# Kernel optimization log

Hardware: AMD Instinct MI355X
Metric: run time of the kernel (lower is better)

Reference implementation:

```python
import jax, jax.numpy as jnp
import numpy as np

B, S, H = 2, 2048, 1024
NH, NKV, HD = 16, 4, 64
Q_SIZE = NH * HD          # 1024
KV_SIZE = NKV * HD        # 256
R_SOFTPLUS_0 = 1.442695041
NEG = -2.3819763e38  # large negative for masking (matches float32 -inf-ish additive mask)


def setup_inputs() -> dict:
    key = jax.random.key(0)
    k1, k2, k3, k4, k5, k6 = jax.random.split(key, 6)
    hidden_states = jax.random.normal(k1, (B, S, H), dtype=jnp.float32)
    # causal additive mask [B, 1, S, S]
    causal = jnp.tril(jnp.ones((S, S), dtype=bool))
    mask = jnp.where(causal, 0.0, NEG).astype(jnp.float32)
    mask = jnp.broadcast_to(mask[None, None], (B, 1, S, S))
    fan = 1.0 / np.sqrt(H)
    qkv_w = jax.random.uniform(k2, ((NH + 2 * NKV) * HD, H), jnp.float32, -fan, fan)
    qkv_b = jax.random.uniform(k3, ((NH + 2 * NKV) * HD,), jnp.float32, -fan, fan)
    fo = 1.0 / np.sqrt(Q_SIZE)
    o_w = jax.random.uniform(k4, (H, Q_SIZE), jnp.float32, -fo, fo)
    o_b = jax.random.uniform(k5, (H,), jnp.float32, -fo, fo)
    scaling = jax.random.normal(k6, (HD,), dtype=jnp.float32)
    return {"hidden_states": hidden_states, "mask": mask, "scaling": scaling,
            "qkv_w": qkv_w, "qkv_b": qkv_b, "o_w": o_w, "o_b": o_b}


def reference(hidden_states, mask, scaling, qkv_w, qkv_b, o_w, o_b):
    b, s, _ = hidden_states.shape
    q_w, k_w, v_w = qkv_w[:Q_SIZE], qkv_w[Q_SIZE:Q_SIZE + KV_SIZE], qkv_w[-KV_SIZE:]
    q_b, k_b, v_b = qkv_b[:Q_SIZE], qkv_b[Q_SIZE:Q_SIZE + KV_SIZE], qkv_b[-KV_SIZE:]
    xq = (hidden_states @ q_w.T + q_b).reshape(b, s, NH, HD)
    # per-dim softplus scaling fused into q
    scale = (R_SOFTPLUS_0 / np.sqrt(HD)) * jax.nn.softplus(scaling)
    xq = xq * scale[None, None, None, :]
    xk = (hidden_states @ k_w.T + k_b).reshape(b, s, NKV, HD)
    xv = (hidden_states @ v_w.T + v_b).reshape(b, s, NKV, HD)
    # GQA: repeat kv heads (repeat_interleave along head dim)
    key = jnp.repeat(xk, NH // NKV, axis=2)   # [b, s, NH, HD]
    value = jnp.repeat(xv, NH // NKV, axis=2)
    scores = jnp.einsum('bqhd,bkhd->bhqk', xq, key) + mask
    scores = jax.nn.softmax(scores.astype(jnp.float32), axis=-1).astype(xq.dtype)
    out = jnp.einsum('bhqk,bkhd->bqhd', scores, value).reshape(b, s, NH * HD)
    out = out @ o_w.T + o_b
    return scores, out
```

## Files before the change

### kernel.cpp

```cpp
#include <hip/hip_runtime.h>
#include <hip/hip_bf16.h>
#include <cstdint>
#include <cstddef>

typedef __attribute__((ext_vector_type(4))) float f32x4;
typedef __attribute__((ext_vector_type(8))) short bf16x8;

#define DEVI static __device__ __forceinline__

DEVI unsigned short f2bf(float f) {
  union { float f; unsigned int u; } v; v.f = f;
  unsigned int u = v.u;
  unsigned int r = (u + 0x7fffu + ((u >> 16) & 1u)) >> 16;
  return (unsigned short)r;
}

DEVI unsigned int cvt_pk(float lo, float hi) {
  unsigned int r;
  asm("v_cvt_pk_bf16_f32 %0, %1, %2" : "=v"(r) : "v"(lo), "v"(hi));
  return r;
}

DEVI f32x4 mfma16(bf16x8 a, bf16x8 b, f32x4 c) {
  return __builtin_amdgcn_mfma_f32_16x16x32_bf16(a, b, c, 0, 0, 0);
}

#define GLDS(gp, lp) __builtin_amdgcn_global_load_lds(                         \
    (const __attribute__((address_space(1))) void*)(const void*)(gp),          \
    (__attribute__((address_space(3))) void*)(void*)(lp), 16, 0, 0)

#define SBAR() asm volatile("s_barrier" ::: "memory")
#define WV(n) asm volatile("s_waitcnt vmcnt(" #n ")" ::: "memory")
#define FORCE4(x) asm volatile("" : "+v"(x))

__global__ void convert_kernel(const float* __restrict__ hidden,
                               const float* __restrict__ qkv_w,
                               const float* __restrict__ o_w,
                               const float* __restrict__ scaling,
                               unsigned short* __restrict__ hbf,
                               unsigned short* __restrict__ wbf,
                               unsigned short* __restrict__ obf,
                               float* __restrict__ qscale) {
  int tid = blockIdx.x * blockDim.x + threadIdx.x;
  int nt = gridDim.x * blockDim.x;
  if (tid < 64) {
    float x = scaling[tid];
    float sp = (x > 20.f) ? x : log1pf(__expf(x));
    qscale[tid] = 0.1803368801243369f * 1.4426950408889634f * sp;
  }
  for (int i = tid; i < 1048576; i += nt) {
    float4 v = ((const float4*)hidden)[i];
    ushort4 o = { f2bf(v.x), f2bf(v.y), f2bf(v.z), f2bf(v.w) };
    ((ushort4*)hbf)[i] = o;
  }
  for (int i = tid; i < 393216; i += nt) {
    float4 v = ((const float4*)qkv_w)[i];
    ushort4 o = { f2bf(v.x), f2bf(v.y), f2bf(v.z), f2bf(v.w) };
    ((ushort4*)wbf)[i] = o;
  }
  for (int i = tid; i < 262144; i += nt) {
    float4 v = ((const float4*)o_w)[i];
    ushort4 o = { f2bf(v.x), f2bf(v.y), f2bf(v.z), f2bf(v.w) };
    ((ushort4*)obf)[i] = o;
  }
}

__global__ __launch_bounds__(256, 2) void gemm_kernel(
    const unsigned short* __restrict__ A,
    const unsigned short* __restrict__ Bw,
    const float* __restrict__ bias,
    const float* __restrict__ qscale,
    unsigned short* __restrict__ oq,
    unsigned short* __restrict__ okv,
    unsigned short* __restrict__ ovt) {
  __shared__ __align__(16) unsigned short sA[128 * 64];
  __shared__ __align__(16) unsigned short sB[128 * 64];
  const int t = threadIdx.x, lane = t & 63, w = t >> 6;
  const int l15 = lane & 15, lg = lane >> 4;
  const int m0 = blockIdx.y * 128, n0 = blockIdx.x * 128;
  const int wr = w >> 1, wc = w & 1;

  f32x4 acc[4][4] = {};

  for (int kb = 0; kb < 1024; kb += 64) {
    __syncthreads();
#pragma unroll
    for (int i = 0; i < 4; i++) {
      int idx = i * 256 + w * 64 + lane;
      int row = idx >> 3;
      int cg = (idx & 7) ^ (row & 7);
      GLDS(A + (size_t)(m0 + row) * 1024 + kb + cg * 8, sA + (i * 256 + w * 64) * 8);
      GLDS(Bw + (size_t)(n0 + row) * 1024 + kb + cg * 8, sB + (i * 256 + w * 64) * 8);
    }
    __syncthreads();
    bf16x8 af[4][2], bfr[4][2];
#pragma unroll
    for (int rt = 0; rt < 4; rt++) {
      int row = wr * 64 + rt * 16 + l15;
#pragma unroll
      for (int kk = 0; kk < 2; kk++) {
        int c = (kk * 4 + lg) ^ (row & 7);
        af[rt][kk] = *(const bf16x8*)((const char*)sA + row * 128 + c * 16);
      }
      int rowb = wc * 64 + rt * 16 + l15;
#pragma unroll
      for (int kk = 0; kk < 2; kk++) {
        int c = (kk * 4 + lg) ^ (rowb & 7);
        bfr[rt][kk] = *(const bf16x8*)((const char*)sB + rowb * 128 + c * 16);
      }
    }
#pragma unroll
    for (int kk = 0; kk < 2; kk++)
#pragma unroll
      for (int rt = 0; rt < 4; rt++)
#pragma unroll
        for (int ct = 0; ct < 4; ct++)
          acc[rt][ct] = mfma16(af[rt][kk], bfr[ct][kk], acc[rt][ct]);
  }

#pragma unroll
  for (int rt = 0; rt < 4; rt++) {
#pragma unroll
    for (int ct = 0; ct < 4; ct++) {
      int n = n0 + wc * 64 + ct * 16 + l15;
      float bv = bias[n];
#pragma unroll
      for (int jj = 0; jj < 4; jj++) {
        int m = m0 + wr * 64 + rt * 16 + lg * 4 + jj;
        float v = acc[rt][ct][jj] + bv;
        int b = m >> 11, s = m & 2047;
        if (n < 1024) {
          int h = n >> 6, d = n & 63;
          v *= qscale[d];
          oq[(((size_t)(b * 16 + h) * 2048 + s) << 6) + d] = f2bf(v);
        } else if (n < 1280) {
          int kv = (n - 1024) >> 6, d = n & 63;
          okv[(((size_t)(b * 4 + kv) * 2048 + s) << 6) + d] = f2bf(v);
        } else {
          int kv = (n - 1280) >> 6, d = n & 63;
          ovt[(((size_t)((b * 4 + kv) * 64 + d)) << 11) + s] = f2bf(v);
        }
      }
    }
  }
}

__global__ __launch_bounds__(256, 2) void gemm2_kernel(
    const unsigned short* __restrict__ A,
    const unsigned short* __restrict__ Bw,
    const float* __restrict__ bias,
    float* __restrict__ of) {
  __shared__ __align__(16) unsigned short sA[64 * 64];
  __shared__ __align__(16) unsigned short sB[128 * 64];
  __shared__ __align__(16) float sT[4][32 * 68];
  const int t = threadIdx.x, lane = t & 63, w = t >> 6;
  const int l15 = lane & 15, lg = lane >> 4;
  const int m0 = blockIdx.y * 64, n0 = blockIdx.x * 128;
  const int wr = w >> 1, wc = w & 1;

  f32x4 acc[2][4] = {};

  for (int kb = 0; kb < 1024; kb += 64) {
    __syncthreads();
#pragma unroll
    for (int i = 0; i < 2; i++) {
      int idx = i * 256 + w * 64 + lane;
      int row = idx >> 3;
      int cg = (idx & 7) ^ (row & 7);
      GLDS(A + (size_t)(m0 + row) * 1024 + kb + cg * 8, sA + (i * 256 + w * 64) * 8);
    }
#pragma unroll
    for (int i = 0; i < 4; i++) {
      int idx = i * 256 + w * 64 + lane;
      int row = idx >> 3;
      int cg = (idx & 7) ^ (row & 7);
      GLDS(Bw + (size_t)(n0 + row) * 1024 + kb + cg * 8, sB + (i * 256 + w * 64) * 8);
    }
    __syncthreads();
    bf16x8 af[2][2], bfr[4][2];
#pragma unroll
    for (int rt = 0; rt < 2; rt++) {
      int row = wr * 32 + rt * 16 + l15;
#pragma unroll
      for (int kk = 0; kk < 2; kk++) {
        int c = (kk * 4 + lg) ^ (row & 7);
        af[rt][kk] = *(const bf16x8*)((const char*)sA + row * 128 + c * 16);
      }
    }
#pragma unroll
    for (int ct = 0; ct < 4; ct++) {
      int rowb = wc * 64 + ct * 16 + l15;
#pragma unroll
      for (int kk = 0; kk < 2; kk++) {
        int c = (kk * 4 + lg) ^ (rowb & 7);
        bfr[ct][kk] = *(const bf16x8*)((const char*)sB + rowb * 128 + c * 16);
      }
    }
#pragma unroll
    for (int kk = 0; kk < 2; kk++)
#pragma unroll
      for (int rt = 0; rt < 2; rt++)
#pragma unroll
        for (int ct = 0; ct < 4; ct++)
          acc[rt][ct] = mfma16(af[rt][kk], bfr[ct][kk], acc[rt][ct]);
  }

#pragma unroll
  for (int rt = 0; rt < 2; rt++)
#pragma unroll
    for (int ct = 0; ct < 4; ct++)
#pragma unroll
      for (int jj = 0; jj < 4; jj++) {
        int r = rt * 16 + lg * 4 + jj;
        int cc = ct * 16 + l15;
        sT[w][r * 68 + cc] = acc[rt][ct][jj];
      }
#pragma unroll
  for (int i = 0; i < 8; i++) {
    int r = i * 4 + lg;
    int cc = l15 * 4;
    f32x4 v = *(const f32x4*)&sT[w][r * 68 + cc];
    int n = n0 + wc * 64 + cc;
    float4 bv = *(const float4*)(bias + n);
    v[0] += bv.x; v[1] += bv.y; v[2] += bv.z; v[3] += bv.w;
    int m = m0 + wr * 32 + r;
    *(f32x4*)(of + (size_t)m * 1024 + n) = v;
  }
}

__global__ __launch_bounds__(256, 2) void attn_kernel(
    const unsigned short* __restrict__ q_ws,
    const unsigned short* __restrict__ k_ws,
    const unsigned short* __restrict__ v_ws,
    float* __restrict__ scores,
    unsigned short* __restrict__ attn_bf) {
  __shared__ __align__(16) unsigned char smem[57344];

  const int t = threadIdx.x, lane = t & 63, w = t >> 6;
  const int l15 = lane & 15, lg = lane >> 4;
  int bid = blockIdx.x;
  int bh = bid & 31;
  int pr = bid >> 5;
  int p = (bid < 256) ? pr : (23 - pr);
  int b = bh >> 4, h = bh & 15, kv = h >> 2;
  const int qtA = p, qtB = 31 - p;
  const int NB = qtB + 1;
  const int start = bid & 15;

  const unsigned short* Kp = k_ws + ((size_t)(b * 4 + kv) * 2048) * 64;
  const unsigned short* Vp = v_ws + ((size_t)(b * 4 + kv) * 64) * 2048;
  const int qrA = qtA * 64 + w * 16 + l15;
  const int qrB = qtB * 64 + w * 16 + l15;

  auto rot = [&](int j) { int n = j + start; return (n >= NB) ? n - NB : n; };
  auto kbuf = [&](int i) { return (unsigned short*)(smem + i * 8192); };
  auto vbuf = [&](int i) { return (unsigned short*)(smem + 32768 + i * 8192); };
  float* Sw = (float*)(smem + 16384 + w * 4096);
  unsigned char* myP = smem + 49152 + w * 2048;

  bf16x8 aqA[2], aqB[2];
  {
    const unsigned short* qa = q_ws + ((size_t)bh * 2048 + qrA) * 64;
    const unsigned short* qb = q_ws + ((size_t)bh * 2048 + qrB) * 64;
    aqA[0] = *(const bf16x8*)(qa + lg * 8);
    aqA[1] = *(const bf16x8*)(qa + 32 + lg * 8);
    aqB[0] = *(const bf16x8*)(qb + lg * 8);
    aqB[1] = *(const bf16x8*)(qb + 32 + lg * 8);
    FORCE4(*(f32x4*)&aqA[0]); FORCE4(*(f32x4*)&aqA[1]);
    FORCE4(*(f32x4*)&aqB[0]); FORCE4(*(f32x4*)&aqB[1]);
  }

  auto stageK = [&](int kt, int bufi) {
#pragma unroll
    for (int i = 0; i < 2; i++) {
      int idx = i * 256 + w * 64 + lane;
      int row = idx >> 3;
      int cg = (idx & 7) ^ (row & 7);
      GLDS(Kp + (size_t)(kt * 64 + row) * 64 + cg * 8, kbuf(bufi) + (i * 256 + w * 64) * 8);
    }
  };
  auto stageVT = [&](int kt, int bufi) {
#pragma unroll
    for (int i = 0; i < 2; i++) {
      int idx = i * 256 + w * 64 + lane;
      int row = idx >> 3;
      int cg = (idx & 7) ^ (row & 7);
      GLDS(Vp + (size_t)row * 2048 + kt * 64 + cg * 8, vbuf(bufi) + (i * 256 + w * 64) * 8);
    }
  };
  auto qk_tile = [&](const unsigned short* kb, const bf16x8(&aq)[2], f32x4(&acc)[4]) {
#pragma unroll
    for (int ct = 0; ct < 4; ct++) {
      int row = ct * 16 + l15;
#pragma unroll
      for (int kk = 0; kk < 2; kk++) {
        int c = (kk * 4 + lg) ^ (row & 7);
        bf16x8 ak = *(const bf16x8*)((const char*)kb + row * 128 + c * 16);
        acc[ct] = mfma16(ak, aq[kk], acc[ct]);
      }
    }
  };
  auto tstore = [&](float* Sp, const f32x4(&acc)[4], int k0) {
#pragma unroll
    for (int ct = 0; ct < 4; ct++) {
      int xs = (ct * 4 + lg) ^ l15;
      *(f32x4*)(Sw + l15 * 64 + xs * 4) = acc[ct];
    }
#pragma unroll
    for (int i = 0; i < 4; i++) {
      int r = i * 4 + lg;
      int xs = l15 ^ r;
      f32x4 v = *(const f32x4*)(Sw + r * 64 + xs * 4);
      *(f32x4*)(Sp + (size_t)(w * 16 + r) * 2048 + k0 + l15 * 4) = v;
    }
  };

  stageK(rot(0), 0);
  stageK(rot(1), 1);
  float rsA = 0.f, rsB = 0.f;
  for (int j = 0; j < NB; j++) {
    const int n = rot(j);
    if (j + 2 < NB) { stageK(rot(j + 2), (j + 2) & 3); WV(4); }
    else if (j + 1 < NB) { WV(2); }
    else { WV(0); }
    SBAR();
    const unsigned short* kb = kbuf(j & 3);
    {
      f32x4 acc[4] = {};
      qk_tile(kb, aqB, acc);
      if (n < NB - 1) {
#pragma unroll
        for (int ct = 0; ct < 4; ct++)
#pragma unroll
          for (int jj = 0; jj < 4; jj++) rsB += __builtin_amdgcn_exp2f(acc[ct][jj]);
      } else {
#pragma unroll
        for (int ct = 0; ct < 4; ct++) {
          int kb0 = n * 64 + ct * 16 + lg * 4;
#pragma unroll
          for (int jj = 0; jj < 4; jj++)
            rsB += (kb0 + jj <= qrB) ? __builtin_amdgcn_exp2f(acc[ct][jj]) : 0.f;
        }
      }
    }
    if (n <= qtA) {
      f32x4 acc[4] = {};
      qk_tile(kb, aqA, acc);
      if (n < qtA) {
#pragma unroll
        for (int ct = 0; ct < 4; ct++)
#pragma unroll
          for (int jj = 0; jj < 4; jj++) rsA += __builtin_amdgcn_exp2f(acc[ct][jj]);
      } else {
#pragma unroll
        for (int ct = 0; ct < 4; ct++) {
          int kb0 = n * 64 + ct * 16 + lg * 4;
#pragma unroll
          for (int jj = 0; jj < 4; jj++)
            rsA += (kb0 + jj <= qrA) ? __builtin_amdgcn_exp2f(acc[ct][jj]) : 0.f;
        }
      }
    }
  }
  rsA += __shfl_xor(rsA, 16); rsA += __shfl_xor(rsA, 32);
  rsB += __shfl_xor(rsB, 16); rsB += __shfl_xor(rsB, 32);
  float rinvA = 1.0f / rsA, rinvB = 1.0f / rsB;

  SBAR();

  stageK(rot(0), 0); stageVT(rot(0), 0);
  f32x4 accoA[4] = {}, accoB[4] = {};
  const int xr = (l15 & 7) << 4;
  float* SpA = scores + ((size_t)bh * 2048 + qtA * 64) * 2048;
  float* SpB = scores + ((size_t)bh * 2048 + qtB * 64) * 2048;

  for (int j = 0; j < NB; j++) {
    const int n = rot(j);
    if (j + 1 < NB) { stageK(rot(j + 1), (j + 1) & 1); stageVT(rot(j + 1), (j + 1) & 1); }
    if (j == 0) { WV(4); }
    else if (j + 1 < NB) { WV(12); }
    else { WV(8); }
    SBAR();
    const unsigned short* kb = kbuf(j & 1);
    const unsigned short* vt = vbuf(j & 1);
    int k0 = n * 64;

    {
      f32x4 acc[4] = {};
      qk_tile(kb, aqB, acc);
      if (n == NB - 1) {
#pragma unroll
        for (int ct = 0; ct < 4; ct++) {
          int kb0 = k0 + ct * 16 + lg * 4;
#pragma unroll
          for (int jj = 0; jj < 4; jj++)
            acc[ct][jj] = (kb0 + jj <= qrB) ? __builtin_amdgcn_exp2f(acc[ct][jj]) * rinvB : 0.f;
        }
      } else {
#pragma unroll
        for (int ct = 0; ct < 4; ct++)
#pragma unroll
          for (int jj = 0; jj < 4; jj++)
            acc[ct][jj] = __builtin_amdgcn_exp2f(acc[ct][jj]) * rinvB;
      }
      tstore(SpB, acc, k0);
#pragma unroll
      for (int ct = 0; ct < 4; ct++) {
        uint2 pw;
        pw.x = cvt_pk(acc[ct][0], acc[ct][1]);
        pw.y = cvt_pk(acc[ct][2], acc[ct][3]);
        *(uint2*)(myP + l15 * 128 + ((ct * 32 + lg * 8) ^ xr)) = pw;
      }
#pragma unroll
      for (int kk = 0; kk < 2; kk++) {
        bf16x8 ap = *(const bf16x8*)(myP + l15 * 128 + ((kk * 64 + lg * 16) ^ xr));
#pragma unroll
        for (int ct = 0; ct < 4; ct++) {
          int vrow = ct * 16 + l15;
          int cv = (kk * 4 + lg) ^ (vrow & 7);
          bf16x8 bv = *(const bf16x8*)((const char*)vt + vrow * 128 + cv * 16);
          accoB[ct] = mfma16(bv, ap, accoB[ct]);
        }
      }
    }

    if (n <= qtA) {
      f32x4 acc[4] = {};
      qk_tile(kb, aqA, acc);
      if (n == qtA) {
#pragma unroll
        for (int ct = 0; ct < 4; ct++) {
          int kb0 = k0 + ct * 16 + lg * 4;
#pragma unroll
          for (int jj = 0; jj < 4; jj++)
            acc[ct][jj] = (kb0 + jj <= qrA) ? __builtin_amdgcn_exp2f(acc[ct][jj]) * rinvA : 0.f;
        }
      } else {
#pragma unroll
        for (int ct = 0; ct < 4; ct++)
#pragma unroll
          for (int jj = 0; jj < 4; jj++)
            acc[ct][jj] = __builtin_amdgcn_exp2f(acc[ct][jj]) * rinvA;
      }
      tstore(SpA, acc, k0);
#pragma unroll
      for (int ct = 0; ct < 4; ct++) {
        uint2 pw;
        pw.x = cvt_pk(acc[ct][0], acc[ct][1]);
        pw.y = cvt_pk(acc[ct][2], acc[ct][3]);
        *(uint2*)(myP + l15 * 128 + ((ct * 32 + lg * 8) ^ xr)) = pw;
      }
#pragma unroll
      for (int kk = 0; kk < 2; kk++) {
        bf16x8 ap = *(const bf16x8*)(myP + l15 * 128 + ((kk * 64 + lg * 16) ^ xr));
#pragma unroll
        for (int ct = 0; ct < 4; ct++) {
          int vrow = ct * 16 + l15;
          int cv = (kk * 4 + lg) ^ (vrow & 7);
          bf16x8 bv = *(const bf16x8*)((const char*)vt + vrow * 128 + cv * 16);
          accoA[ct] = mfma16(bv, ap, accoA[ct]);
        }
      }
    } else {
      f32x4 z = {0.f, 0.f, 0.f, 0.f};
#pragma unroll
      for (int i = 0; i < 4; i++) {
        int r = i * 4 + lg;
        *(f32x4*)(SpA + (size_t)(w * 16 + r) * 2048 + k0 + l15 * 4) = z;
      }
    }
    SBAR();
  }

  {
    int mA = b * 2048 + qtA * 64 + w * 16 + l15;
    int mB = b * 2048 + qtB * 64 + w * 16 + l15;
    unsigned int* oA = (unsigned int*)(attn_bf + (size_t)mA * 1024 + h * 64);
    unsigned int* oB = (unsigned int*)(attn_bf + (size_t)mB * 1024 + h * 64);
#pragma unroll
    for (int ct = 0; ct < 4; ct++) {
      uint2 pa, pb;
      pa.x = cvt_pk(accoA[ct][0], accoA[ct][1]);
      pa.y = cvt_pk(accoA[ct][2], accoA[ct][3]);
      pb.x = cvt_pk(accoB[ct][0], accoB[ct][1]);
      pb.y = cvt_pk(accoB[ct][2], accoB[ct][3]);
      *(uint2*)(oA + (ct * 16 + lg * 4) / 2) = pa;
      *(uint2*)(oB + (ct * 16 + lg * 4) / 2) = pb;
    }
  }

  int zbase = NB * 64;
  if (zbase < 2048) {
    f32x4 z = {0.f, 0.f, 0.f, 0.f};
    for (int c0 = zbase; c0 < 2048; c0 += 64) {
#pragma unroll
      for (int i = 0; i < 4; i++) {
        int r = i * 4 + lg;
        *(f32x4*)(SpA + (size_t)(w * 16 + r) * 2048 + c0 + l15 * 4) = z;
        *(f32x4*)(SpB + (size_t)(w * 16 + r) * 2048 + c0 + l15 * 4) = z;
      }
    }
  }
}

extern "C" void kernel_launch(void* const* d_in, const int* in_sizes, int n_in,
                              void* d_out, int out_size, void* d_ws, size_t ws_size,
                              hipStream_t stream) {
  const float* hidden  = (const float*)d_in[0];
  const float* scaling = (const float*)d_in[2];
  const float* qkv_w   = (const float*)d_in[3];
  const float* qkv_b   = (const float*)d_in[4];
  const float* o_w     = (const float*)d_in[5];
  const float* o_b     = (const float*)d_in[6];

  float* scores = (float*)d_out;
  float* outp   = (float*)d_out + (size_t)2 * 16 * 2048 * 2048;

  char* ws = (char*)d_ws;
  unsigned short* hidden_bf = (unsigned short*)(ws + 0);
  unsigned short* qkvw_bf   = (unsigned short*)(ws + 8388608);
  unsigned short* ow_bf     = (unsigned short*)(ws + 11534336);
  unsigned short* q_ws      = (unsigned short*)(ws + 13631488);
  unsigned short* k_ws      = (unsigned short*)(ws + 22020096);
  unsigned short* v_ws      = (unsigned short*)(ws + 24117248);
  unsigned short* attn_bf   = (unsigned short*)(ws + 26214400);
  float* qscale             = (float*)(ws + 34603008);

  convert_kernel<<<512, 256, 0, stream>>>(hidden, qkv_w, o_w, scaling,
                                          hidden_bf, qkvw_bf, ow_bf, qscale);
  gemm_kernel<<<dim3(12, 32), 256, 0, stream>>>(hidden_bf, qkvw_bf, qkv_b,
                                                qscale, q_ws, k_ws, v_ws);
  attn_kernel<<<512, 256, 0, stream>>>(q_ws, k_ws, v_ws, scores, attn_bf);
  gemm2_kernel<<<dim3(8, 64), 256, 0, stream>>>(attn_bf, ow_bf, o_b, outp);
}
```

Baseline: 189.5 us.

## Retile QKV GEMM to 64x192 blocks and share K fragments across query tiles

The QKV projection GEMM moves from 128x128 tiles on a 12x32 grid to 64x192 tiles on an 8x64 grid, with each wave covering all 64 rows and a 48-column slice. This raises the block count from 384 to 512 to fill the CUs better, at the cost of less A reuse per block. In the attention kernel, a new qk_tile2 loads each K fragment from LDS once and feeds it to the MFMAs for both query tiles A and B. That removes duplicate LDS reads when both tiles are active, but keeps two accumulator sets live at once, which adds register pressure.

```diff
diff --git a/kernel.cpp b/kernel.cpp
--- a/kernel.cpp
+++ b/kernel.cpp
@@ -73,40 +73,48 @@
     unsigned short* __restrict__ oq,
     unsigned short* __restrict__ okv,
     unsigned short* __restrict__ ovt) {
-  __shared__ __align__(16) unsigned short sA[128 * 64];
-  __shared__ __align__(16) unsigned short sB[128 * 64];
+  __shared__ __align__(16) unsigned short sA[64 * 64];
+  __shared__ __align__(16) unsigned short sB[192 * 64];
   const int t = threadIdx.x, lane = t & 63, w = t >> 6;
   const int l15 = lane & 15, lg = lane >> 4;
-  const int m0 = blockIdx.y * 128, n0 = blockIdx.x * 128;
-  const int wr = w >> 1, wc = w & 1;
-
-  f32x4 acc[4][4] = {};
+  const int m0 = blockIdx.y * 64, n0 = blockIdx.x * 192;
+
+  f32x4 acc[4][3] = {};
 
   for (int kb = 0; kb < 1024; kb += 64) {
     __syncthreads();
 #pragma unroll
-    for (int i = 0; i < 4; i++) {
+    for (int i = 0; i < 2; i++) {
       int idx = i * 256 + w * 64 + lane;
       int row = idx >> 3;
       int cg = (idx & 7) ^ (row & 7);
       GLDS(A + (size_t)(m0 + row) * 1024 + kb + cg * 8, sA + (i * 256 + w * 64) * 8);
+    }
+#pragma unroll
+    for (int i = 0; i < 6; i++) {
+      int idx = i * 256 + w * 64 + lane;
+      int row = idx >> 3;
+      int cg = (idx & 7) ^ (row & 7);
       GLDS(Bw + (size_t)(n0 + row) * 1024 + kb + cg * 8, sB + (i * 256 + w * 64) * 8);
     }
     __syncthreads();
-    bf16x8 af[4][2], bfr[4][2];
+    bf16x8 af[4][2], bfr[3][2];
 #pragma unroll
     for (int rt = 0; rt < 4; rt++) {
-      int row = wr * 64 + rt * 16 + l15;
+      int row = rt * 16 + l15;
 #pragma unroll
       for (int kk = 0; kk < 2; kk++) {
         int c = (kk * 4 + lg) ^ (row & 7);
         af[rt][kk] = *(const bf16x8*)((const char*)sA + row * 128 + c * 16);
       }
-      int rowb = wc * 64 + rt * 16 + l15;
+    }
+#pragma unroll
+    for (int ct = 0; ct < 3; ct++) {
+      int rowb = w * 48 + ct * 16 + l15;
 #pragma unroll
       for (int kk = 0; kk < 2; kk++) {
         int c = (kk * 4 + lg) ^ (rowb & 7);
-        bfr[rt][kk] = *(const bf16x8*)((const char*)sB + rowb * 128 + c * 16);
+        bfr[ct][kk] = *(const bf16x8*)((const char*)sB + rowb * 128 + c * 16);
       }
     }
 #pragma unroll
@@ -114,19 +122,19 @@
 #pragma unroll
       for (int rt = 0; rt < 4; rt++)
 #pragma unroll
-        for (int ct = 0; ct < 4; ct++)
+        for (int ct = 0; ct < 3; ct++)
           acc[rt][ct] = mfma16(af[rt][kk], bfr[ct][kk], acc[rt][ct]);
   }
 
 #pragma unroll
   for (int rt = 0; rt < 4; rt++) {
 #pragma unroll
-    for (int ct = 0; ct < 4; ct++) {
-      int n = n0 + wc * 64 + ct * 16 + l15;
+    for (int ct = 0; ct < 3; ct++) {
+      int n = n0 + w * 48 + ct * 16 + l15;
       float bv = bias[n];
 #pragma unroll
       for (int jj = 0; jj < 4; jj++) {
-        int m = m0 + wr * 64 + rt * 16 + lg * 4 + jj;
+        int m = m0 + rt * 16 + lg * 4 + jj;
         float v = acc[rt][ct][jj] + bv;
         int b = m >> 11, s = m & 2047;
         if (n < 1024) {
@@ -300,6 +308,19 @@
       }
     }
   };
+  auto qk_tile2 = [&](const unsigned short* kb, f32x4(&accB)[4], f32x4(&accA)[4]) {
+#pragma unroll
+    for (int ct = 0; ct < 4; ct++) {
+      int row = ct * 16 + l15;
+#pragma unroll
+      for (int kk = 0; kk < 2; kk++) {
+        int c = (kk * 4 + lg) ^ (row & 7);
+        bf16x8 ak = *(const bf16x8*)((const char*)kb + row * 128 + c * 16);
+        accB[ct] = mfma16(ak, aqB[kk], accB[ct]);
+        accA[ct] = mfma16(ak, aqA[kk], accA[ct]);
+      }
+    }
+  };
   auto tstore = [&](float* Sp, const f32x4(&acc)[4], int k0) {
 #pragma unroll
     for (int ct = 0; ct < 4; ct++) {
@@ -325,39 +346,36 @@
     else { WV(0); }
     SBAR();
     const unsigned short* kb = kbuf(j & 3);
-    {
-      f32x4 acc[4] = {};
-      qk_tile(kb, aqB, acc);
-      if (n < NB - 1) {
+    const bool doA = (n <= qtA);
+    f32x4 aB4[4] = {}, aA4[4] = {};
+    if (doA) { qk_tile2(kb, aB4, aA4); } else { qk_tile(kb, aqB, aB4); }
+    if (n < NB - 1) {
+#pragma unroll
+      for (int ct = 0; ct < 4; ct++)
+#pragma unroll
+        for (int jj = 0; jj < 4; jj++) rsB += __builtin_amdgcn_exp2f(aB4[ct][jj]);
+    } else {
+#pragma unroll
+      for (int ct = 0; ct < 4; ct++) {
+        int kb0 = n * 64 + ct * 16 + lg * 4;
+#pragma unroll
+        for (int jj = 0; jj < 4; jj++)
+          rsB += (kb0 + jj <= qrB) ? __builtin_amdgcn_exp2f(aB4[ct][jj]) : 0.f;
+      }
+    }
+    if (doA) {
+      if (n < qtA) {
 #pragma unroll
         for (int ct = 0; ct < 4; ct++)
 #pragma unroll
-          for (int jj = 0; jj < 4; jj++) rsB += __builtin_amdgcn_exp2f(acc[ct][jj]);
+          for (int jj = 0; jj < 4; jj++) rsA += __builtin_amdgcn_exp2f(aA4[ct][jj]);
       } else {
 #pragma unroll
         for (int ct = 0; ct < 4; ct++) {
           int kb0 = n * 64 + ct * 16 + lg * 4;
 #pragma unroll
           for (int jj = 0; jj < 4; jj++)
-            rsB += (kb0 + jj <= qrB) ? __builtin_amdgcn_exp2f(acc[ct][jj]) : 0.f;
-        }
-      }
-    }
-    if (n <= qtA) {
-      f32x4 acc[4] = {};
-      qk_tile(kb, aqA, acc);
-      if (n < qtA) {
-#pragma unroll
-        for (int ct = 0; ct < 4; ct++)
-#pragma unroll
-          for (int jj = 0; jj < 4; jj++) rsA += __builtin_amdgcn_exp2f(acc[ct][jj]);
-      } else {
-#pragma unroll
-        for (int ct = 0; ct < 4; ct++) {
-          int kb0 = n * 64 + ct * 16 + lg * 4;
-#pragma unroll
-          for (int jj = 0; jj < 4; jj++)
-            rsA += (kb0 + jj <= qrA) ? __builtin_amdgcn_exp2f(acc[ct][jj]) : 0.f;
+            rsA += (kb0 + jj <= qrA) ? __builtin_amdgcn_exp2f(aA4[ct][jj]) : 0.f;
         }
       }
     }
@@ -384,31 +402,33 @@
     const unsigned short* kb = kbuf(j & 1);
     const unsigned short* vt = vbuf(j & 1);
     int k0 = n * 64;
+    const bool doA = (n <= qtA);
+
+    f32x4 aB4[4] = {}, aA4[4] = {};
+    if (doA) { qk_tile2(kb, aB4, aA4); } else { qk_tile(kb, aqB, aB4); }
 
     {
-      f32x4 acc[4] = {};
-      qk_tile(kb, aqB, acc);
       if (n == NB - 1) {
 #pragma unroll
         for (int ct = 0; ct < 4; ct++) {
           int kb0 = k0 + ct * 16 + lg * 4;
 #pragma unroll
           for (int jj = 0; jj < 4; jj++)
-            acc[ct][jj] = (kb0 + jj <= qrB) ? __builtin_amdgcn_exp2f(acc[ct][jj]) * rinvB : 0.f;
+            aB4[ct][jj] = (kb0 + jj <= qrB) ? __builtin_amdgcn_exp2f(aB4[ct][jj]) * rinvB : 0.f;
         }
       } else {
 #pragma unroll
         for (int ct = 0; ct < 4; ct++)
 #pragma unroll
           for (int jj = 0; jj < 4; jj++)
-            acc[ct][jj] = __builtin_amdgcn_exp2f(acc[ct][jj]) * rinvB;
-      }
-      tstore(SpB, acc, k0);
+            aB4[ct][jj] = __builtin_amdgcn_exp2f(aB4[ct][jj]) * rinvB;
+      }
+      tstore(SpB, aB4, k0);
 #pragma unroll
       for (int ct = 0; ct < 4; ct++) {
         uint2 pw;
-        pw.x = cvt_pk(acc[ct][0], acc[ct][1]);
-        pw.y = cvt_pk(acc[ct][2], acc[ct][3]);
+        pw.x = cvt_pk(aB4[ct][0], aB4[ct][1]);
+        pw.y = cvt_pk(aB4[ct][2], aB4[ct][3]);
         *(uint2*)(myP + l15 * 128 + ((ct * 32 + lg * 8) ^ xr)) = pw;
       }
 #pragma unroll
@@ -424,30 +444,28 @@
       }
     }
 
-    if (n <= qtA) {
-      f32x4 acc[4] = {};
-      qk_tile(kb, aqA, acc);
+    if (doA) {
       if (n == qtA) {
 #pragma unroll
         for (int ct = 0; ct < 4; ct++) {
           int kb0 = k0 + ct * 16 + lg * 4;
 #pragma unroll
           for (int jj = 0; jj < 4; jj++)
-            acc[ct][jj] = (kb0 + jj <= qrA) ? __builtin_amdgcn_exp2f(acc[ct][jj]) * rinvA : 0.f;
+            aA4[ct][jj] = (kb0 + jj <= qrA) ? __builtin_amdgcn_exp2f(aA4[ct][jj]) * rinvA : 0.f;
         }
       } else {
 #pragma unroll
         for (int ct = 0; ct < 4; ct++)
 #pragma unroll
           for (int jj = 0; jj < 4; jj++)
-            acc[ct][jj] = __builtin_amdgcn_exp2f(acc[ct][jj]) * rinvA;
-      }
-      tstore(SpA, acc, k0);
+            aA4[ct][jj] = __builtin_amdgcn_exp2f(aA4[ct][jj]) * rinvA;
+      }
+      tstore(SpA, aA4, k0);
 #pragma unroll
       for (int ct = 0; ct < 4; ct++) {
         uint2 pw;
-        pw.x = cvt_pk(acc[ct][0], acc[ct][1]);
-        pw.y = cvt_pk(acc[ct][2], acc[ct][3]);
+        pw.x = cvt_pk(aA4[ct][0], aA4[ct][1]);
+        pw.y = cvt_pk(aA4[ct][2], aA4[ct][3]);
         *(uint2*)(myP + l15 * 128 + ((ct * 32 + lg * 8) ^ xr)) = pw;
       }
 #pragma unroll
@@ -528,8 +546,8 @@
 
   convert_kernel<<<512, 256, 0, stream>>>(hidden, qkv_w, o_w, scaling,
                                           hidden_bf, qkvw_bf, ow_bf, qscale);
-  gemm_kernel<<<dim3(12, 32), 256, 0, stream>>>(hidden_bf, qkvw_bf, qkv_b,
-                                                qscale, q_ws, k_ws, v_ws);
+  gemm_kernel<<<dim3(8, 64), 256, 0, stream>>>(hidden_bf, qkvw_bf, qkv_b,
+                                               qscale, q_ws, k_ws, v_ws);
   attn_kernel<<<512, 256, 0, stream>>>(q_ws, k_ws, v_ws, scores, attn_bf);
   gemm2_kernel<<<dim3(8, 64), 256, 0, stream>>>(attn_bf, ow_bf, o_b, outp);
 }
```

Result: faster. 183.2 us (-3.3%).
